# Kernel tuning notes

Measured on AMD Instinct MI355X. Metric: run time of the kernel, lower is better.

## Reference

```python
import jax, jax.numpy as jnp
import numpy as np

B, C, P = 32, 192, 3136
EPS = 0.01


def setup_inputs() -> dict:
    key = jax.random.key(0)
    k1, k2, k3 = jax.random.split(key, 3)
    return {
        "embeddings": jax.random.normal(k1, (B, C, P), dtype=jnp.float32),
        "means": jax.random.normal(k2, (P, C), dtype=jnp.float32),
        "covariances": jax.random.normal(k3, (P, C, C), dtype=jnp.float32),
        "n": 96,
    }


def reference(embeddings, means, covariances, n):
    # embeddings: [B, C, P]; means: [P, C] (running sums); covariances: [P, C, C] (running outer-product sums)
    b = embeddings.shape[0]
    c = embeddings.shape[1]
    # Training-branch accumulation: per-patch sum of outer products over the batch,
    # expressed as one batched GEMM instead of P*B tiny torch.outer calls.
    new_means = means + jnp.einsum("bcp->pc", embeddings)
    new_covs = covariances + jnp.einsum("bcp,bdp->pcd", embeddings, embeddings)
    n_new = n + b
    # calculate_means_and_covariances(): finalize sample mean / covariance per patch.
    learned_means = new_means / n_new  # [P, C]
    learned_covs = (new_covs - n_new * jnp.einsum("pc,pd->pcd", learned_means, learned_means)) / (n_new - 1)
    learned_covs = learned_covs + EPS * jnp.eye(c, dtype=learned_covs.dtype)
    return (learned_means, learned_covs)
```

## Files before the change

### kernel.cpp

```cpp
#include <hip/hip_runtime.h>


#define BB 32
#define CC 192
#define PP 3136
#define II (BB * CC)
#define EPSV 0.01f
#define WROW 52

typedef float f32x4 __attribute__((ext_vector_type(4)));
typedef short bf16x8 __attribute__((ext_vector_type(8)));

__device__ __forceinline__ unsigned short f2bf(float f) {
    unsigned int u = __float_as_uint(f);
    u += 0x7fffu + ((u >> 16) & 1u);
    return (unsigned short)(u >> 16);
}
__device__ __forceinline__ float bflo(unsigned int u) { return __uint_as_float(u << 16); }
__device__ __forceinline__ float bfhi(unsigned int u) { return __uint_as_float(u & 0xffff0000u); }

__global__ __launch_bounds__(256) void transpose_bf16(
    const float* __restrict__ emb, unsigned short* __restrict__ Et)
{
    __shared__ unsigned short tile[512 * 34];
    const int c0 = blockIdx.x * 16;
    const int p0 = blockIdx.y * 32;
    const int t = threadIdx.x;
    const int tc = t & 31;
    const int rg = t >> 5;

    #pragma unroll 8
    for (int k = 0; k < 64; ++k) {
        const int r = k * 8 + rg;
        const int b = r & 31;
        const int cl = r >> 5;
        const float v = __builtin_nontemporal_load(
            &emb[(size_t)(b * CC + c0 + cl) * PP + (p0 + tc)]);
        tile[r * 34 + tc] = f2bf(v);
    }
    __syncthreads();

    const int pl = t >> 3;
    unsigned short* dst = Et + (size_t)(p0 + pl) * II + c0 * 32;
    #pragma unroll
    for (int w = 0; w < 8; ++w) {
        const int q = w * 8 + (t & 7);
        const int rbase = (q >> 2) * 32 + (q & 3) * 8;
        unsigned int dw[4];
        #pragma unroll
        for (int j = 0; j < 4; ++j) {
            const unsigned int lo = tile[(rbase + 2 * j) * 34 + pl];
            const unsigned int hi = tile[(rbase + 2 * j + 1) * 34 + pl];
            dw[j] = lo | (hi << 16);
        }
        uint4 val; val.x = dw[0]; val.y = dw[1]; val.z = dw[2]; val.w = dw[3];
        *reinterpret_cast<uint4*>(dst + q * 8) = val;
    }
}

__global__ __launch_bounds__(256, 3) void padim_mfma(
    const unsigned short* __restrict__ Et,
    const float* __restrict__ means,
    const float* __restrict__ covs,
    const int*   __restrict__ n_ptr,
    float* __restrict__ out_means,
    float* __restrict__ out_covs)
{
    __shared__ float m_lds[CC];
    __shared__ __align__(16) float wbuf[4][2][16 * WROW];

    const int bid = blockIdx.x;
    const int u = (bid & 7) * (PP * 2 / 8) + (bid >> 3);
    const int slab = u & 1;
    const int p = u >> 1;

    const int t = threadIdx.x;
    const int lane = t & 63;
    const int w = t >> 6;
    const int l15 = lane & 15;
    const int l4  = lane >> 4;

    const float n_new = (float)(n_ptr[0] + BB);
    const float inv_nnew = 1.0f / n_new;
    const float inv_nm1 = 1.0f / (n_new - 1.0f);

    const unsigned short* __restrict__ Erow = Et + (size_t)p * II;

    bf16x8 Af[3], Bf[6];
    #pragma unroll
    for (int dt = 0; dt < 3; ++dt) {
        const int rA = (3 * w + dt) * 16 + l15;
        Af[dt] = *reinterpret_cast<const bf16x8*>(Erow + rA * 32 + l4 * 8);
    }
    #pragma unroll
    for (int ct = 0; ct < 6; ++ct) {
        const int rB = (slab * 6 + ct) * 16 + l15;
        Bf[ct] = *reinterpret_cast<const bf16x8*>(Erow + rB * 32 + l4 * 8);
    }

    if (t < CC) {
        const uint4* rp = reinterpret_cast<const uint4*>(Erow + t * 32);
        float s = 0.f;
        #pragma unroll
        for (int q = 0; q < 4; ++q) {
            const uint4 v = rp[q];
            s += bflo(v.x) + bfhi(v.x) + bflo(v.y) + bfhi(v.y)
               + bflo(v.z) + bfhi(v.z) + bflo(v.w) + bfhi(v.w);
        }
        const float mm = (means[(size_t)p * CC + t] + s) * inv_nnew;
        m_lds[t] = mm;
        if (slab == 0) out_means[(size_t)p * CC + t] = mm;
    }
    __syncthreads();

    f32x4 acc[3][6];
    #pragma unroll
    for (int dt = 0; dt < 3; ++dt)
        #pragma unroll
        for (int ct = 0; ct < 6; ++ct)
            acc[dt][ct] = (f32x4){0.f, 0.f, 0.f, 0.f};

    #pragma unroll
    for (int ct = 0; ct < 6; ++ct)
        #pragma unroll
        for (int dt = 0; dt < 3; ++dt)
            acc[dt][ct] = __builtin_amdgcn_mfma_f32_16x16x32_bf16(
                Af[dt], Bf[ct], acc[dt][ct], 0, 0, 0);

    const float* __restrict__ cov_p = covs + (size_t)p * CC * CC;
    float* __restrict__ out_p = out_covs + (size_t)p * CC * CC;

    int rk[3], qk[3];
    f32x4 mdk[3];
    size_t offb[3];
    #pragma unroll
    for (int k = 0; k < 3; ++k) {
        const int chunk = k * 64 + lane;
        rk[k] = chunk / 12;
        qk[k] = chunk - rk[k] * 12;
        mdk[k] = *reinterpret_cast<const f32x4*>(&m_lds[48 * w + 4 * qk[k]]);
        offb[k] = (size_t)rk[k] * CC + 48 * w + 4 * qk[k];
    }

    #pragma unroll
    for (int ct = 0; ct < 6; ++ct) {
        const int cbase = (slab * 6 + ct) * 16;
        float* buf = &wbuf[w][ct & 1][0];

        f32x4 cin[3];
        #pragma unroll
        for (int k = 0; k < 3; ++k)
            cin[k] = *reinterpret_cast<const f32x4*>(cov_p + (size_t)cbase * CC + offb[k]);

        #pragma unroll
        for (int dt = 0; dt < 3; ++dt)
            *reinterpret_cast<f32x4*>(&buf[l15 * WROW + (dt * 4 + l4) * 4]) = acc[dt][ct];

        #pragma unroll
        for (int k = 0; k < 3; ++k) {
            const f32x4 a = *reinterpret_cast<const f32x4*>(&buf[rk[k] * WROW + 4 * qk[k]]);
            const int c = cbase + rk[k];
            const float nmc = n_new * m_lds[c];
            f32x4 o = (cin[k] + a - nmc * mdk[k]) * inv_nm1;
            const int dd = c - (48 * w + 4 * qk[k]);
            o.x += (dd == 0) ? EPSV : 0.f;
            o.y += (dd == 1) ? EPSV : 0.f;
            o.z += (dd == 2) ? EPSV : 0.f;
            o.w += (dd == 3) ? EPSV : 0.f;
            *reinterpret_cast<f32x4*>(out_p + (size_t)cbase * CC + offb[k]) = o;
        }
    }
}

__global__ __launch_bounds__(256, 3) void padim_fallback(
    const float* __restrict__ emb, const float* __restrict__ means,
    const float* __restrict__ covs, const int* __restrict__ n_ptr,
    float* __restrict__ out_means, float* __restrict__ out_covs)
{
    __shared__ __align__(16) float E[II];
    __shared__ __align__(16) float m[CC];
    const int bid = blockIdx.x;
    const int p = (bid & 7) * (PP / 8) + (bid >> 3);
    const int t = threadIdx.x;
    const float n_new = (float)(n_ptr[0] + BB);
    const float inv_nnew = 1.0f / n_new;
    const float inv_nm1 = 1.0f / (n_new - 1.0f);
    #pragma unroll
    for (int k = 0; k < II / 256; ++k) {
        const int i = t + k * 256;
        E[i] = emb[(size_t)i * PP + p];
    }
    __syncthreads();
    if (t < CC) {
        float s = 0.0f;
        #pragma unroll
        for (int b = 0; b < BB; ++b) s += E[b * CC + t];
        const float mm = (means[(size_t)p * CC + t] + s) * inv_nnew;
        m[t] = mm;
        out_means[(size_t)p * CC + t] = mm;
    }
    __syncthreads();
    const int tx = t & 15, ty = t >> 4;
    const int dbase0 = tx * 4;
    const float* __restrict__ cov_p = covs + (size_t)p * CC * CC;
    float* __restrict__ out_p = out_covs + (size_t)p * CC * CC;
    float md[12];
    *reinterpret_cast<float4*>(&md[0]) = *reinterpret_cast<const float4*>(&m[dbase0]);
    *reinterpret_cast<float4*>(&md[4]) = *reinterpret_cast<const float4*>(&m[64 + dbase0]);
    *reinterpret_cast<float4*>(&md[8]) = *reinterpret_cast<const float4*>(&m[128 + dbase0]);
    #pragma unroll
    for (int pass = 0; pass < 2; ++pass) {
        const int c0 = pass * 96 + ty * 6;
        float acc[6][12];
        #pragma unroll
        for (int i = 0; i < 6; ++i)
            #pragma unroll
            for (int j = 0; j < 12; ++j) acc[i][j] = 0.f;
        #pragma unroll 4
        for (int b = 0; b < BB; ++b) {
            const float* __restrict__ Eb = E + b * CC;
            float cs[6], ds[12];
            *reinterpret_cast<float4*>(&ds[0]) = *reinterpret_cast<const float4*>(&Eb[dbase0]);
            *reinterpret_cast<float4*>(&ds[4]) = *reinterpret_cast<const float4*>(&Eb[64 + dbase0]);
            *reinterpret_cast<float4*>(&ds[8]) = *reinterpret_cast<const float4*>(&Eb[128 + dbase0]);
            *reinterpret_cast<float2*>(&cs[0]) = *reinterpret_cast<const float2*>(&Eb[c0]);
            *reinterpret_cast<float2*>(&cs[2]) = *reinterpret_cast<const float2*>(&Eb[c0 + 2]);
            *reinterpret_cast<float2*>(&cs[4]) = *reinterpret_cast<const float2*>(&Eb[c0 + 4]);
            #pragma unroll
            for (int i = 0; i < 6; ++i)
                #pragma unroll
                for (int j = 0; j < 12; ++j)
                    acc[i][j] = fmaf(cs[i], ds[j], acc[i][j]);
        }
        float mc[6];
        *reinterpret_cast<float2*>(&mc[0]) = *reinterpret_cast<const float2*>(&m[c0]);
        *reinterpret_cast<float2*>(&mc[2]) = *reinterpret_cast<const float2*>(&m[c0 + 2]);
        *reinterpret_cast<float2*>(&mc[4]) = *reinterpret_cast<const float2*>(&m[c0 + 4]);
        #pragma unroll
        for (int i = 0; i < 6; ++i) {
            const int c = c0 + i;
            const size_t row = (size_t)c * CC;
            const float nmc = n_new * mc[i];
            #pragma unroll
            for (int g = 0; g < 3; ++g) {
                const int db = g * 64 + dbase0;
                const float4 cin = *reinterpret_cast<const float4*>(&cov_p[row + db]);
                float4 o;
                o.x = (cin.x + acc[i][g*4+0] - nmc * md[g*4+0]) * inv_nm1;
                o.y = (cin.y + acc[i][g*4+1] - nmc * md[g*4+1]) * inv_nm1;
                o.z = (cin.z + acc[i][g*4+2] - nmc * md[g*4+2]) * inv_nm1;
                o.w = (cin.w + acc[i][g*4+3] - nmc * md[g*4+3]) * inv_nm1;
                const int dd = c - db;
                if (dd == 0) o.x += EPSV;
                if (dd == 1) o.y += EPSV;
                if (dd == 2) o.z += EPSV;
                if (dd == 3) o.w += EPSV;
                *reinterpret_cast<float4*>(&out_p[row + db]) = o;
            }
        }
    }
}

extern "C" void kernel_launch(void* const* d_in, const int* in_sizes, int n_in,
                              void* d_out, int out_size, void* d_ws, size_t ws_size,
                              hipStream_t stream) {
    const float* emb   = (const float*)d_in[0];
    const float* means = (const float*)d_in[1];
    const float* covs  = (const float*)d_in[2];
    const int*   n_ptr = (const int*)d_in[3];

    float* out_means = (float*)d_out;
    float* out_covs  = (float*)d_out + (size_t)PP * CC;

    const size_t et_bytes = (size_t)PP * II * sizeof(unsigned short);
    if (ws_size >= et_bytes) {
        unsigned short* Et = (unsigned short*)d_ws;
        hipLaunchKernelGGL(transpose_bf16, dim3(CC / 16, PP / 32), dim3(256),
                           0, stream, emb, Et);
        hipLaunchKernelGGL(padim_mfma, dim3(PP * 2), dim3(256), 0, stream,
                           Et, means, covs, n_ptr, out_means, out_covs);
    } else {
        hipLaunchKernelGGL(padim_fallback, dim3(PP), dim3(256), 0, stream,
                           emb, means, covs, n_ptr, out_means, out_covs);
    }
}
```

Before: 219.1 us.

## Move mean computation into transpose kernel and prefetch covariance loads ahead

The per-patch mean reduction moves into the transpose kernel, which reads the LDS tile it already holds and writes the finalized means. The MFMA kernel then reads those means from global memory, which removes its LDS mean buffer and the block-wide barrier. Covariance input tiles are now issued with nontemporal loads before and during the MFMA/epilogue loop, so their memory latency overlaps compute. The cost is many more live registers (cin[6][3], mck), which could reduce occupancy.

```diff
diff --git a/kernel.cpp b/kernel.cpp
--- a/kernel.cpp
+++ b/kernel.cpp
@@ -16,11 +16,14 @@
     u += 0x7fffu + ((u >> 16) & 1u);
     return (unsigned short)(u >> 16);
 }
-__device__ __forceinline__ float bflo(unsigned int u) { return __uint_as_float(u << 16); }
-__device__ __forceinline__ float bfhi(unsigned int u) { return __uint_as_float(u & 0xffff0000u); }
+__device__ __forceinline__ float bf16val(unsigned short u) {
+    return __uint_as_float(((unsigned int)u) << 16);
+}
 
 __global__ __launch_bounds__(256) void transpose_bf16(
-    const float* __restrict__ emb, unsigned short* __restrict__ Et)
+    const float* __restrict__ emb, const float* __restrict__ means,
+    const int* __restrict__ n_ptr,
+    unsigned short* __restrict__ Et, float* __restrict__ out_means)
 {
     __shared__ unsigned short tile[512 * 34];
     const int c0 = blockIdx.x * 16;
@@ -40,33 +43,50 @@
     }
     __syncthreads();
 
-    const int pl = t >> 3;
-    unsigned short* dst = Et + (size_t)(p0 + pl) * II + c0 * 32;
-    #pragma unroll
-    for (int w = 0; w < 8; ++w) {
-        const int q = w * 8 + (t & 7);
-        const int rbase = (q >> 2) * 32 + (q & 3) * 8;
-        unsigned int dw[4];
-        #pragma unroll
-        for (int j = 0; j < 4; ++j) {
-            const unsigned int lo = tile[(rbase + 2 * j) * 34 + pl];
-            const unsigned int hi = tile[(rbase + 2 * j + 1) * 34 + pl];
-            dw[j] = lo | (hi << 16);
-        }
-        uint4 val; val.x = dw[0]; val.y = dw[1]; val.z = dw[2]; val.w = dw[3];
-        *reinterpret_cast<uint4*>(dst + q * 8) = val;
+    {
+        const int pl = t >> 3;
+        unsigned short* dst = Et + (size_t)(p0 + pl) * II + c0 * 32;
+        #pragma unroll
+        for (int w = 0; w < 8; ++w) {
+            const int q = w * 8 + (t & 7);
+            const int rbase = (q >> 2) * 32 + (q & 3) * 8;
+            unsigned int dw[4];
+            #pragma unroll
+            for (int j = 0; j < 4; ++j) {
+                const unsigned int lo = tile[(rbase + 2 * j) * 34 + pl];
+                const unsigned int hi = tile[(rbase + 2 * j + 1) * 34 + pl];
+                dw[j] = lo | (hi << 16);
+            }
+            uint4 val; val.x = dw[0]; val.y = dw[1]; val.z = dw[2]; val.w = dw[3];
+            *reinterpret_cast<uint4*>(dst + q * 8) = val;
+        }
+    }
+
+    {
+        const float n_new = (float)(n_ptr[0] + BB);
+        const float inv_nnew = 1.0f / n_new;
+        const int cl = t >> 4;
+        const int ph = t & 15;
+        #pragma unroll
+        for (int h = 0; h < 2; ++h) {
+            const int pp = ph + 16 * h;
+            float s = 0.f;
+            #pragma unroll
+            for (int b = 0; b < 32; ++b)
+                s += bf16val(tile[(cl * 32 + b) * 34 + pp]);
+            const size_t idx = (size_t)(p0 + pp) * CC + (c0 + cl);
+            out_means[idx] = (means[idx] + s) * inv_nnew;
+        }
     }
 }
 
 __global__ __launch_bounds__(256, 3) void padim_mfma(
     const unsigned short* __restrict__ Et,
-    const float* __restrict__ means,
+    const float* __restrict__ lmeans,
     const float* __restrict__ covs,
     const int*   __restrict__ n_ptr,
-    float* __restrict__ out_means,
     float* __restrict__ out_covs)
 {
-    __shared__ float m_lds[CC];
     __shared__ __align__(16) float wbuf[4][2][16 * WROW];
 
     const int bid = blockIdx.x;
@@ -81,7 +101,6 @@
     const int l4  = lane >> 4;
 
     const float n_new = (float)(n_ptr[0] + BB);
-    const float inv_nnew = 1.0f / n_new;
     const float inv_nm1 = 1.0f / (n_new - 1.0f);
 
     const unsigned short* __restrict__ Erow = Et + (size_t)p * II;
@@ -98,38 +117,7 @@
         Bf[ct] = *reinterpret_cast<const bf16x8*>(Erow + rB * 32 + l4 * 8);
     }
 
-    if (t < CC) {
-        const uint4* rp = reinterpret_cast<const uint4*>(Erow + t * 32);
-        float s = 0.f;
-        #pragma unroll
-        for (int q = 0; q < 4; ++q) {
-            const uint4 v = rp[q];
-            s += bflo(v.x) + bfhi(v.x) + bflo(v.y) + bfhi(v.y)
-               + bflo(v.z) + bfhi(v.z) + bflo(v.w) + bfhi(v.w);
-        }
-        const float mm = (means[(size_t)p * CC + t] + s) * inv_nnew;
-        m_lds[t] = mm;
-        if (slab == 0) out_means[(size_t)p * CC + t] = mm;
-    }
-    __syncthreads();
-
-    f32x4 acc[3][6];
-    #pragma unroll
-    for (int dt = 0; dt < 3; ++dt)
-        #pragma unroll
-        for (int ct = 0; ct < 6; ++ct)
-            acc[dt][ct] = (f32x4){0.f, 0.f, 0.f, 0.f};
-
-    #pragma unroll
-    for (int ct = 0; ct < 6; ++ct)
-        #pragma unroll
-        for (int dt = 0; dt < 3; ++dt)
-            acc[dt][ct] = __builtin_amdgcn_mfma_f32_16x16x32_bf16(
-                Af[dt], Bf[ct], acc[dt][ct], 0, 0, 0);
-
-    const float* __restrict__ cov_p = covs + (size_t)p * CC * CC;
-    float* __restrict__ out_p = out_covs + (size_t)p * CC * CC;
-
+    const float* __restrict__ mrow = lmeans + (size_t)p * CC;
     int rk[3], qk[3];
     f32x4 mdk[3];
     size_t offb[3];
@@ -138,19 +126,51 @@
         const int chunk = k * 64 + lane;
         rk[k] = chunk / 12;
         qk[k] = chunk - rk[k] * 12;
-        mdk[k] = *reinterpret_cast<const f32x4*>(&m_lds[48 * w + 4 * qk[k]]);
+        mdk[k] = *reinterpret_cast<const f32x4*>(&mrow[48 * w + 4 * qk[k]]);
         offb[k] = (size_t)rk[k] * CC + 48 * w + 4 * qk[k];
     }
+    float mck[6][3];
+    #pragma unroll
+    for (int ct = 0; ct < 6; ++ct)
+        #pragma unroll
+        for (int k = 0; k < 3; ++k)
+            mck[ct][k] = mrow[(slab * 6 + ct) * 16 + rk[k]];
+
+    const float* __restrict__ cov_p = covs + (size_t)p * CC * CC;
+    float* __restrict__ out_p = out_covs + (size_t)p * CC * CC;
+
+    f32x4 cin[6][3];
+    #pragma unroll
+    for (int ct = 0; ct < 3; ++ct)
+        #pragma unroll
+        for (int k = 0; k < 3; ++k)
+            cin[ct][k] = __builtin_nontemporal_load(reinterpret_cast<const f32x4*>(
+                cov_p + (size_t)((slab * 6 + ct) * 16) * CC + offb[k]));
+
+    f32x4 acc[3][6];
+    #pragma unroll
+    for (int dt = 0; dt < 3; ++dt)
+        #pragma unroll
+        for (int ct = 0; ct < 6; ++ct)
+            acc[dt][ct] = (f32x4){0.f, 0.f, 0.f, 0.f};
+
+    #pragma unroll
+    for (int ct = 0; ct < 6; ++ct)
+        #pragma unroll
+        for (int dt = 0; dt < 3; ++dt)
+            acc[dt][ct] = __builtin_amdgcn_mfma_f32_16x16x32_bf16(
+                Af[dt], Bf[ct], acc[dt][ct], 0, 0, 0);
 
     #pragma unroll
     for (int ct = 0; ct < 6; ++ct) {
+        if (ct + 3 < 6) {
+            #pragma unroll
+            for (int k = 0; k < 3; ++k)
+                cin[ct + 3][k] = __builtin_nontemporal_load(reinterpret_cast<const f32x4*>(
+                    cov_p + (size_t)((slab * 6 + ct + 3) * 16) * CC + offb[k]));
+        }
         const int cbase = (slab * 6 + ct) * 16;
         float* buf = &wbuf[w][ct & 1][0];
-
-        f32x4 cin[3];
-        #pragma unroll
-        for (int k = 0; k < 3; ++k)
-            cin[k] = *reinterpret_cast<const f32x4*>(cov_p + (size_t)cbase * CC + offb[k]);
 
         #pragma unroll
         for (int dt = 0; dt < 3; ++dt)
@@ -160,8 +180,8 @@
         for (int k = 0; k < 3; ++k) {
             const f32x4 a = *reinterpret_cast<const f32x4*>(&buf[rk[k] * WROW + 4 * qk[k]]);
             const int c = cbase + rk[k];
-            const float nmc = n_new * m_lds[c];
-            f32x4 o = (cin[k] + a - nmc * mdk[k]) * inv_nm1;
+            const float nmc = n_new * mck[ct][k];
+            f32x4 o = (cin[ct][k] + a - nmc * mdk[k]) * inv_nm1;
             const int dd = c - (48 * w + 4 * qk[k]);
             o.x += (dd == 0) ? EPSV : 0.f;
             o.y += (dd == 1) ? EPSV : 0.f;
@@ -276,9 +296,9 @@
     if (ws_size >= et_bytes) {
         unsigned short* Et = (unsigned short*)d_ws;
         hipLaunchKernelGGL(transpose_bf16, dim3(CC / 16, PP / 32), dim3(256),
-                           0, stream, emb, Et);
+                           0, stream, emb, means, n_ptr, Et, out_means);
         hipLaunchKernelGGL(padim_mfma, dim3(PP * 2), dim3(256), 0, stream,
-                           Et, means, covs, n_ptr, out_means, out_covs);
+                           Et, out_means, covs, n_ptr, out_covs);
     } else {
         hipLaunchKernelGGL(padim_fallback, dim3(PP), dim3(256), 0, stream,
                            emb, means, covs, n_ptr, out_means, out_covs);
```

Result: slower. 225.6 us (+3.0%).
